# Kernel tuning notes

Hardware: AMD Instinct MI355X
Metric: run time of the kernel (lower is better)

Reference implementation:

```python
import jax, jax.numpy as jnp
import numpy as np

HID = 1024

def setup_inputs() -> dict:
    key = jax.random.key(0)
    k1, k2, k3, k4, k5 = jax.random.split(key, 5)
    B, S, H = 16, 2048, HID
    queries = jax.random.normal(k1, (B, H), dtype=jnp.float32)
    keys = jax.random.normal(k2, (B, S, H), dtype=jnp.float32)
    values = jax.random.normal(k3, (B, S, H), dtype=jnp.float32)
    # additive_attention params: Linear(2H->H), ReLU, Linear(H->1)
    s1 = 1.0 / np.sqrt(2 * H)
    s2 = 1.0 / np.sqrt(H)
    W1 = jax.random.uniform(k4, (2 * H, H), dtype=jnp.float32, minval=-s1, maxval=s1)
    b1 = jnp.zeros((H,), dtype=jnp.float32)
    W2 = jax.random.uniform(k5, (H, 1), dtype=jnp.float32, minval=-s2, maxval=s2)
    b2 = jnp.zeros((1,), dtype=jnp.float32)
    return {"queries": queries, "keys": keys, "values": values,
            "W1": W1, "b1": b1, "W2": W2, "b2": b2}

def reference(queries, keys, values, W1, b1, W2, b2):
    B, S, H = keys.shape
    # concat expanded query with keys along feature dim: [B,S,2H]
    q_exp = jnp.broadcast_to(queries[:, None, :], (B, S, H))
    concat = jnp.concatenate([q_exp, keys], axis=-1)
    h = jax.nn.relu(jnp.einsum('bsf,fh->bsh', concat, W1) + b1)
    scores = jnp.einsum('bsh,ho->bso', h, W2) + b2          # [B,S,1]
    alphas = jax.nn.softmax(scores, axis=1)                  # softmax over seq
    # context = alphas^T @ values : [B,1,H]
    context = jnp.einsum('bso,bsh->boh', alphas, values)
    return (context, alphas)
```

## Files before the change

kernel.cpp:

```cpp
#include <hip/hip_runtime.h>

#define HID 1024
#define SEQ 2048
#define NB  16

typedef __attribute__((ext_vector_type(8))) short bf16x8;
typedef __attribute__((ext_vector_type(4))) float f32x4;

static __device__ __forceinline__ short f2bf(float f) {
    union { float f; unsigned u; } v; v.f = f;
    unsigned u = v.u + 0x7fffu + ((v.u >> 16) & 1u);
    return (short)(u >> 16);
}
static __device__ __forceinline__ unsigned pk2(float a, float b) {
    return (unsigned)(unsigned short)f2bf(a) | ((unsigned)(unsigned short)f2bf(b) << 16);
}
static __device__ __forceinline__ void glds16(const void* g, void* l) {
    __builtin_amdgcn_global_load_lds(
        (const __attribute__((address_space(1))) unsigned*)g,
        (__attribute__((address_space(3))) unsigned*)l, 16, 0, 0);
}

__global__ __launch_bounds__(256) void prep_all(const float* __restrict__ keys,
                                                short* __restrict__ kbf,
                                                const float* __restrict__ W1,
                                                const float* __restrict__ queries,
                                                const float* __restrict__ b1,
                                                short* __restrict__ w1t,
                                                float* __restrict__ qproj,
                                                int nconv) {
    __shared__ float shmem[2048];
    const int tid = threadIdx.x;
    int bw = blockIdx.x;

    if (bw < 32) {
        const int f0 = (bw >> 2) * 128;
        const int n0 = (bw & 3) * 256;
#pragma unroll
        for (int j = 0; j < 8; ++j) {
            const int idx = tid * 8 + j;
            const int b = idx >> 7, f = idx & 127;
            shmem[idx] = queries[b * HID + f0 + f];
        }
        __syncthreads();
        float acc[16];
        const float bv = (bw >> 2 == 0) ? b1[n0 + tid] : 0.0f;
#pragma unroll
        for (int b = 0; b < 16; ++b) acc[b] = (b == 0) ? bv : 0.0f;
        if (bw >> 2 == 0) {
#pragma unroll
            for (int b = 1; b < 16; ++b) acc[b] = bv;
        }
        for (int f = 0; f < 128; ++f) {
            const float w = W1[(size_t)(f0 + f) * HID + n0 + tid];
#pragma unroll
            for (int b = 0; b < 16; ++b)
                acc[b] += shmem[b * 128 + f] * w;
        }
#pragma unroll
        for (int b = 0; b < 16; ++b)
            atomicAdd(&qproj[b * HID + n0 + tid], acc[b]);
        return;
    }
    bw -= 32;
    if (bw < 1024) {
        float (*t)[33] = (float(*)[33])shmem;
        const int k0 = (bw & 31) * 32;
        const int n0 = (bw >> 5) * 32;
        const int tx = tid & 31, ty = tid >> 5;
#pragma unroll
        for (int i = 0; i < 32; i += 8)
            t[ty + i][tx] = W1[(size_t)(HID + k0 + ty + i) * HID + n0 + tx];
        __syncthreads();
#pragma unroll
        for (int i = 0; i < 32; i += 8)
            w1t[(size_t)(n0 + ty + i) * HID + k0 + tx] = f2bf(t[tx][ty + i]);
        return;
    }
    bw -= 1024;
    if (bw < nconv) {
        const size_t i = ((size_t)bw * 256 + tid) * 8;
        const float4 a = *(const float4*)(keys + i);
        const float4 b = *(const float4*)(keys + i + 4);
        int4 o;
        o.x = (int)pk2(a.x, a.y); o.y = (int)pk2(a.z, a.w);
        o.z = (int)pk2(b.x, b.y); o.w = (int)pk2(b.z, b.w);
        *(int4*)(kbf + i) = o;
    }
}

template<int PRE>
__global__ __launch_bounds__(256) void score_gemm128(const float* __restrict__ keys,
                                                     const short* __restrict__ kbf,
                                                     const short* __restrict__ w1t,
                                                     const float* __restrict__ qproj,
                                                     const float* __restrict__ W2,
                                                     float* __restrict__ scores) {
    __shared__ short As[128 * 32];
    __shared__ short Bs[128 * 32];

    const int tid  = threadIdx.x;
    const int lane = tid & 63;
    const int wave = tid >> 6;
    const int n0 = blockIdx.x * 128;
    const int m0 = blockIdx.y * 128;
    const int batch = m0 >> 11;
    const int wm = wave >> 1, wn = wave & 1;
    const int q = lane >> 4, c = lane & 15;

    const int lrow = lane >> 2;
    const int lk   = (lane & 3) * 8;

    f32x4 acc[4][4] = {};

    for (int k0 = 0; k0 < HID; k0 += 32) {
#pragma unroll
        for (int call = 0; call < 2; ++call) {
            const int rbase = (wave * 2 + call) * 16;
            glds16(w1t + (size_t)(n0 + rbase + lrow) * HID + k0 + lk,
                   &Bs[rbase * 32]);
        }
        if (PRE) {
#pragma unroll
            for (int call = 0; call < 2; ++call) {
                const int rbase = (wave * 2 + call) * 16;
                glds16(kbf + (size_t)(m0 + rbase + lrow) * HID + k0 + lk,
                       &As[rbase * 32]);
            }
        } else {
            const int r = tid >> 1, h = (tid & 1) * 16;
            const float* src = keys + (size_t)(m0 + r) * HID + k0 + h;
            const float4 v0 = *(const float4*)(src + 0);
            const float4 v1 = *(const float4*)(src + 4);
            const float4 v2 = *(const float4*)(src + 8);
            const float4 v3 = *(const float4*)(src + 12);
            int4 o0, o1;
            o0.x = (int)pk2(v0.x, v0.y); o0.y = (int)pk2(v0.z, v0.w);
            o0.z = (int)pk2(v1.x, v1.y); o0.w = (int)pk2(v1.z, v1.w);
            o1.x = (int)pk2(v2.x, v2.y); o1.y = (int)pk2(v2.z, v2.w);
            o1.z = (int)pk2(v3.x, v3.y); o1.w = (int)pk2(v3.z, v3.w);
            *(int4*)&As[r * 32 + h + 0] = o0;
            *(int4*)&As[r * 32 + h + 8] = o1;
        }
        __syncthreads();

        bf16x8 af[4], bf[4];
#pragma unroll
        for (int i = 0; i < 4; ++i)
            af[i] = *(const bf16x8*)&As[(wm * 64 + i * 16 + c) * 32 + q * 8];
#pragma unroll
        for (int i = 0; i < 4; ++i)
            bf[i] = *(const bf16x8*)&Bs[(wn * 64 + i * 16 + c) * 32 + q * 8];
#pragma unroll
        for (int mi = 0; mi < 4; ++mi)
#pragma unroll
            for (int ni = 0; ni < 4; ++ni)
                acc[mi][ni] = __builtin_amdgcn_mfma_f32_16x16x32_bf16(af[mi], bf[ni], acc[mi][ni], 0, 0, 0);
        __syncthreads();
    }

    const float* qp = qproj + batch * HID + n0 + wn * 64;
    const float* w2 = W2 + n0 + wn * 64;
    float psum[4][4] = {};
#pragma unroll
    for (int ni = 0; ni < 4; ++ni) {
        const float qv = qp[ni * 16 + c];
        const float wv = w2[ni * 16 + c];
#pragma unroll
        for (int mi = 0; mi < 4; ++mi)
#pragma unroll
            for (int r = 0; r < 4; ++r)
                psum[mi][r] += fmaxf(acc[mi][ni][r] + qv, 0.f) * wv;
    }
#pragma unroll
    for (int m = 1; m < 16; m <<= 1)
#pragma unroll
        for (int mi = 0; mi < 4; ++mi)
#pragma unroll
            for (int r = 0; r < 4; ++r)
                psum[mi][r] += __shfl_xor(psum[mi][r], m, 64);
    if (c == 0) {
#pragma unroll
        for (int mi = 0; mi < 4; ++mi) {
            const int row = m0 + wm * 64 + mi * 16 + q * 4;
#pragma unroll
            for (int r = 0; r < 4; ++r)
                atomicAdd(&scores[row + r], psum[mi][r]);
        }
    }
}

__global__ __launch_bounds__(256) void softmax_k(const float* __restrict__ scores,
                                                 float* __restrict__ alphas,
                                                 float* __restrict__ ctx) {
    __shared__ float red[256];
    const int b = blockIdx.x;
    const int tid = threadIdx.x;
    float4 z = {0.f, 0.f, 0.f, 0.f};
    *(float4*)(ctx + b * HID + tid * 4) = z;

    float loc[8];
    float mx = -1e30f;
#pragma unroll
    for (int i = 0; i < 8; ++i) {
        loc[i] = scores[b * SEQ + tid + i * 256];
        mx = fmaxf(mx, loc[i]);
    }
    red[tid] = mx; __syncthreads();
    for (int s = 128; s > 0; s >>= 1) {
        if (tid < s) red[tid] = fmaxf(red[tid], red[tid + s]);
        __syncthreads();
    }
    mx = red[0]; __syncthreads();
    float sum = 0.f;
#pragma unroll
    for (int i = 0; i < 8; ++i) { loc[i] = expf(loc[i] - mx); sum += loc[i]; }
    red[tid] = sum; __syncthreads();
    for (int s = 128; s > 0; s >>= 1) {
        if (tid < s) red[tid] += red[tid + s];
        __syncthreads();
    }
    const float inv = 1.0f / red[0];
#pragma unroll
    for (int i = 0; i < 8; ++i) alphas[b * SEQ + tid + i * 256] = loc[i] * inv;
}

__global__ __launch_bounds__(256) void context_k(const float* __restrict__ alphas,
                                                 const float* __restrict__ values,
                                                 float* __restrict__ context) {
    const int b = blockIdx.y;
    const int s0 = blockIdx.x * 64;
    const int col = threadIdx.x * 4;
    float4 acc = {0.f, 0.f, 0.f, 0.f};
    for (int i = 0; i < 64; ++i) {
        const int s = s0 + i;
        const float a = alphas[b * SEQ + s];
        const float4 v = *(const float4*)(values + (size_t)(b * SEQ + s) * HID + col);
        acc.x += a * v.x; acc.y += a * v.y; acc.z += a * v.z; acc.w += a * v.w;
    }
    float* cp = context + b * HID + col;
    atomicAdd(cp + 0, acc.x);
    atomicAdd(cp + 1, acc.y);
    atomicAdd(cp + 2, acc.z);
    atomicAdd(cp + 3, acc.w);
}

extern "C" void kernel_launch(void* const* d_in, const int* in_sizes, int n_in,
                              void* d_out, int out_size, void* d_ws, size_t ws_size,
                              hipStream_t stream) {
    const float* queries = (const float*)d_in[0];
    const float* keys    = (const float*)d_in[1];
    const float* values  = (const float*)d_in[2];
    const float* W1      = (const float*)d_in[3];
    const float* b1      = (const float*)d_in[4];
    const float* W2      = (const float*)d_in[5];

    float* out_ctx   = (float*)d_out;
    float* out_alpha = (float*)d_out + NB * HID;

    char* ws = (char*)d_ws;
    float* scores = (float*)ws;
    float* qproj  = (float*)(ws + 131072);
    short* w1t    = (short*)(ws + 196608);
    short* kbf    = (short*)(ws + 2293760);

    const size_t need_pre = 2293760ull + 67108864ull;
    const bool pre = ws_size >= need_pre;
    const int nconv = pre ? 16384 : 0;

    hipMemsetAsync(ws, 0, 196608, stream);

    prep_all<<<32 + 1024 + nconv, 256, 0, stream>>>(
        keys, kbf, W1, queries, b1, w1t, qproj, nconv);

    if (pre)
        score_gemm128<1><<<dim3(8, 256), 256, 0, stream>>>(keys, kbf, w1t, qproj, W2, scores);
    else
        score_gemm128<0><<<dim3(8, 256), 256, 0, stream>>>(keys, kbf, w1t, qproj, W2, scores);

    softmax_k<<<NB, 256, 0, stream>>>(scores, out_alpha, out_ctx);
    context_k<<<dim3(32, NB), 256, 0, stream>>>(out_alpha, values, out_ctx);
}
```

Measured before the change: 382.8 us.

## Fuse key bf16 conversion into score GEMM with full-row LDS tiles

Drops the separate pass that converts keys to bf16 in workspace. Each 512-thread block now loads 64 full key rows, converts them to bf16 into a swizzled 128KB LDS tile, and computes all 1024 hidden columns. W1^T fragments are read straight from global memory without LDS staging. Scores are reduced across waves in shared memory and written directly, replacing the atomics and the memset of the score buffer. context_k also caches alphas in LDS. The tradeoff is one block per CU at most, given the LDS size, and B operands read from global each k-step.

```diff
diff --git a/kernel.cpp b/kernel.cpp
--- a/kernel.cpp
+++ b/kernel.cpp
@@ -15,20 +15,12 @@
 static __device__ __forceinline__ unsigned pk2(float a, float b) {
     return (unsigned)(unsigned short)f2bf(a) | ((unsigned)(unsigned short)f2bf(b) << 16);
 }
-static __device__ __forceinline__ void glds16(const void* g, void* l) {
-    __builtin_amdgcn_global_load_lds(
-        (const __attribute__((address_space(1))) unsigned*)g,
-        (__attribute__((address_space(3))) unsigned*)l, 16, 0, 0);
-}
-
-__global__ __launch_bounds__(256) void prep_all(const float* __restrict__ keys,
-                                                short* __restrict__ kbf,
-                                                const float* __restrict__ W1,
+
+__global__ __launch_bounds__(256) void prep_all(const float* __restrict__ W1,
                                                 const float* __restrict__ queries,
                                                 const float* __restrict__ b1,
                                                 short* __restrict__ w1t,
-                                                float* __restrict__ qproj,
-                                                int nconv) {
+                                                float* __restrict__ qproj) {
     __shared__ float shmem[2048];
     const int tid = threadIdx.x;
     int bw = blockIdx.x;
@@ -46,11 +38,7 @@
         float acc[16];
         const float bv = (bw >> 2 == 0) ? b1[n0 + tid] : 0.0f;
 #pragma unroll
-        for (int b = 0; b < 16; ++b) acc[b] = (b == 0) ? bv : 0.0f;
-        if (bw >> 2 == 0) {
-#pragma unroll
-            for (int b = 1; b < 16; ++b) acc[b] = bv;
-        }
+        for (int b = 0; b < 16; ++b) acc[b] = bv;
         for (int f = 0; f < 128; ++f) {
             const float w = W1[(size_t)(f0 + f) * HID + n0 + tid];
 #pragma unroll
@@ -63,7 +51,7 @@
         return;
     }
     bw -= 32;
-    if (bw < 1024) {
+    {
         float (*t)[33] = (float(*)[33])shmem;
         const int k0 = (bw & 31) * 32;
         const int n0 = (bw >> 5) * 32;
@@ -75,103 +63,75 @@
 #pragma unroll
         for (int i = 0; i < 32; i += 8)
             w1t[(size_t)(n0 + ty + i) * HID + k0 + tx] = f2bf(t[tx][ty + i]);
-        return;
-    }
-    bw -= 1024;
-    if (bw < nconv) {
-        const size_t i = ((size_t)bw * 256 + tid) * 8;
-        const float4 a = *(const float4*)(keys + i);
-        const float4 b = *(const float4*)(keys + i + 4);
-        int4 o;
-        o.x = (int)pk2(a.x, a.y); o.y = (int)pk2(a.z, a.w);
-        o.z = (int)pk2(b.x, b.y); o.w = (int)pk2(b.z, b.w);
-        *(int4*)(kbf + i) = o;
-    }
-}
-
-template<int PRE>
-__global__ __launch_bounds__(256) void score_gemm128(const float* __restrict__ keys,
-                                                     const short* __restrict__ kbf,
-                                                     const short* __restrict__ w1t,
-                                                     const float* __restrict__ qproj,
-                                                     const float* __restrict__ W2,
-                                                     float* __restrict__ scores) {
-    __shared__ short As[128 * 32];
-    __shared__ short Bs[128 * 32];
+    }
+}
+
+__global__ __launch_bounds__(512, 2) void score_fused(const float* __restrict__ keys,
+                                                      const short* __restrict__ w1t,
+                                                      const float* __restrict__ qproj,
+                                                      const float* __restrict__ W2,
+                                                      float* __restrict__ scores) {
+    __shared__ __align__(16) short A[64 * HID];
+    __shared__ float red[8][64];
 
     const int tid  = threadIdx.x;
     const int lane = tid & 63;
     const int wave = tid >> 6;
-    const int n0 = blockIdx.x * 128;
-    const int m0 = blockIdx.y * 128;
+    const int c = lane & 15, q = lane >> 4;
+    const int m0 = blockIdx.x * 64;
     const int batch = m0 >> 11;
-    const int wm = wave >> 1, wn = wave & 1;
-    const int q = lane >> 4, c = lane & 15;
-
-    const int lrow = lane >> 2;
-    const int lk   = (lane & 3) * 8;
-
-    f32x4 acc[4][4] = {};
-
-    for (int k0 = 0; k0 < HID; k0 += 32) {
-#pragma unroll
-        for (int call = 0; call < 2; ++call) {
-            const int rbase = (wave * 2 + call) * 16;
-            glds16(w1t + (size_t)(n0 + rbase + lrow) * HID + k0 + lk,
-                   &Bs[rbase * 32]);
-        }
-        if (PRE) {
-#pragma unroll
-            for (int call = 0; call < 2; ++call) {
-                const int rbase = (wave * 2 + call) * 16;
-                glds16(kbf + (size_t)(m0 + rbase + lrow) * HID + k0 + lk,
-                       &As[rbase * 32]);
-            }
-        } else {
-            const int r = tid >> 1, h = (tid & 1) * 16;
-            const float* src = keys + (size_t)(m0 + r) * HID + k0 + h;
-            const float4 v0 = *(const float4*)(src + 0);
-            const float4 v1 = *(const float4*)(src + 4);
-            const float4 v2 = *(const float4*)(src + 8);
-            const float4 v3 = *(const float4*)(src + 12);
-            int4 o0, o1;
-            o0.x = (int)pk2(v0.x, v0.y); o0.y = (int)pk2(v0.z, v0.w);
-            o0.z = (int)pk2(v1.x, v1.y); o0.w = (int)pk2(v1.z, v1.w);
-            o1.x = (int)pk2(v2.x, v2.y); o1.y = (int)pk2(v2.z, v2.w);
-            o1.z = (int)pk2(v3.x, v3.y); o1.w = (int)pk2(v3.z, v3.w);
-            *(int4*)&As[r * 32 + h + 0] = o0;
-            *(int4*)&As[r * 32 + h + 8] = o1;
-        }
-        __syncthreads();
-
-        bf16x8 af[4], bf[4];
-#pragma unroll
-        for (int i = 0; i < 4; ++i)
-            af[i] = *(const bf16x8*)&As[(wm * 64 + i * 16 + c) * 32 + q * 8];
-#pragma unroll
-        for (int i = 0; i < 4; ++i)
-            bf[i] = *(const bf16x8*)&Bs[(wn * 64 + i * 16 + c) * 32 + q * 8];
-#pragma unroll
-        for (int mi = 0; mi < 4; ++mi)
+
+#pragma unroll
+    for (int it = 0; it < 16; ++it) {
+        const int idx  = it * 512 + tid;
+        const int row  = idx >> 7;
+        const int slot = idx & 127;
+        const float* src = keys + (size_t)(m0 + row) * HID + slot * 8;
+        const float4 v0 = *(const float4*)src;
+        const float4 v1 = *(const float4*)(src + 4);
+        int4 o;
+        o.x = (int)pk2(v0.x, v0.y); o.y = (int)pk2(v0.z, v0.w);
+        o.z = (int)pk2(v1.x, v1.y); o.w = (int)pk2(v1.z, v1.w);
+        *(int4*)&A[row * HID + ((slot ^ (row & 7)) << 3)] = o;
+    }
+    __syncthreads();
+
+    const int xr = c & 7;
+    float psum[4][4] = {};
+
+#pragma unroll 1
+    for (int g = 0; g < 2; ++g) {
+        const int nb = wave * 128 + g * 64;
+        f32x4 acc[4][4] = {};
+        const short* b0 = w1t + (size_t)(nb + c) * HID + q * 8;
+#pragma unroll
+        for (int k0 = 0; k0 < HID; k0 += 32) {
+            bf16x8 bf[4], af[4];
 #pragma unroll
             for (int ni = 0; ni < 4; ++ni)
-                acc[mi][ni] = __builtin_amdgcn_mfma_f32_16x16x32_bf16(af[mi], bf[ni], acc[mi][ni], 0, 0, 0);
-        __syncthreads();
-    }
-
-    const float* qp = qproj + batch * HID + n0 + wn * 64;
-    const float* w2 = W2 + n0 + wn * 64;
-    float psum[4][4] = {};
-#pragma unroll
-    for (int ni = 0; ni < 4; ++ni) {
-        const float qv = qp[ni * 16 + c];
-        const float wv = w2[ni * 16 + c];
-#pragma unroll
-        for (int mi = 0; mi < 4; ++mi)
-#pragma unroll
-            for (int r = 0; r < 4; ++r)
-                psum[mi][r] += fmaxf(acc[mi][ni][r] + qv, 0.f) * wv;
-    }
+                bf[ni] = *(const bf16x8*)(b0 + ni * 16 * HID + k0);
+#pragma unroll
+            for (int mi = 0; mi < 4; ++mi)
+                af[mi] = *(const bf16x8*)&A[(mi * 16 + c) * HID + ((((k0 >> 3) + q) ^ xr) << 3)];
+#pragma unroll
+            for (int mi = 0; mi < 4; ++mi)
+#pragma unroll
+                for (int ni = 0; ni < 4; ++ni)
+                    acc[mi][ni] = __builtin_amdgcn_mfma_f32_16x16x32_bf16(af[mi], bf[ni], acc[mi][ni], 0, 0, 0);
+        }
+#pragma unroll
+        for (int ni = 0; ni < 4; ++ni) {
+            const int n = nb + ni * 16 + c;
+            const float qv = qproj[batch * HID + n];
+            const float wv = W2[n];
+#pragma unroll
+            for (int mi = 0; mi < 4; ++mi)
+#pragma unroll
+                for (int r = 0; r < 4; ++r)
+                    psum[mi][r] += fmaxf(acc[mi][ni][r] + qv, 0.f) * wv;
+        }
+    }
+
 #pragma unroll
     for (int m = 1; m < 16; m <<= 1)
 #pragma unroll
@@ -181,12 +141,17 @@
                 psum[mi][r] += __shfl_xor(psum[mi][r], m, 64);
     if (c == 0) {
 #pragma unroll
-        for (int mi = 0; mi < 4; ++mi) {
-            const int row = m0 + wm * 64 + mi * 16 + q * 4;
+        for (int mi = 0; mi < 4; ++mi)
 #pragma unroll
             for (int r = 0; r < 4; ++r)
-                atomicAdd(&scores[row + r], psum[mi][r]);
-        }
+                red[wave][mi * 16 + q * 4 + r] = psum[mi][r];
+    }
+    __syncthreads();
+    if (tid < 64) {
+        float s = 0.f;
+#pragma unroll
+        for (int w = 0; w < 8; ++w) s += red[w][tid];
+        scores[m0 + tid] = s;
     }
 }
 
@@ -228,14 +193,18 @@
 __global__ __launch_bounds__(256) void context_k(const float* __restrict__ alphas,
                                                  const float* __restrict__ values,
                                                  float* __restrict__ context) {
+    __shared__ float al[64];
     const int b = blockIdx.y;
     const int s0 = blockIdx.x * 64;
-    const int col = threadIdx.x * 4;
+    const int tid = threadIdx.x;
+    if (tid < 64) al[tid] = alphas[b * SEQ + s0 + tid];
+    __syncthreads();
+    const int col = tid * 4;
     float4 acc = {0.f, 0.f, 0.f, 0.f};
+#pragma unroll 4
     for (int i = 0; i < 64; ++i) {
-        const int s = s0 + i;
-        const float a = alphas[b * SEQ + s];
-        const float4 v = *(const float4*)(values + (size_t)(b * SEQ + s) * HID + col);
+        const float a = al[i];
+        const float4 v = *(const float4*)(values + (size_t)(b * SEQ + s0 + i) * HID + col);
         acc.x += a * v.x; acc.y += a * v.y; acc.z += a * v.z; acc.w += a * v.w;
     }
     float* cp = context + b * HID + col;
@@ -262,21 +231,12 @@
     float* scores = (float*)ws;
     float* qproj  = (float*)(ws + 131072);
     short* w1t    = (short*)(ws + 196608);
-    short* kbf    = (short*)(ws + 2293760);
-
-    const size_t need_pre = 2293760ull + 67108864ull;
-    const bool pre = ws_size >= need_pre;
-    const int nconv = pre ? 16384 : 0;
-
-    hipMemsetAsync(ws, 0, 196608, stream);
-
-    prep_all<<<32 + 1024 + nconv, 256, 0, stream>>>(
-        keys, kbf, W1, queries, b1, w1t, qproj, nconv);
-
-    if (pre)
-        score_gemm128<1><<<dim3(8, 256), 256, 0, stream>>>(keys, kbf, w1t, qproj, W2, scores);
-    else
-        score_gemm128<0><<<dim3(8, 256), 256, 0, stream>>>(keys, kbf, w1t, qproj, W2, scores);
+
+    hipMemsetAsync(ws + 131072, 0, 65536, stream);
+
+    prep_all<<<32 + 1024, 256, 0, stream>>>(W1, queries, b1, w1t, qproj);
+
+    score_fused<<<512, 512, 0, stream>>>(keys, w1t, qproj, W2, scores);
 
     softmax_k<<<NB, 256, 0, stream>>>(scores, out_alpha, out_ctx);
     context_k<<<dim3(32, NB), 256, 0, stream>>>(out_alpha, values, out_ctx);
```

Measured after the change: 633.6 us. +65.5%, slower.
